# Kernel tuning notes

Hardware: AMD Instinct MI355X
Metric: run time of the kernel (lower is better)

The kernel has to match this reference:

```python
import jax, jax.numpy as jnp
import numpy as np

# (dy, dx) offsets corresponding to the single -1 entries of kernels 1..8
# delta1 rows: (0,0),(0,1),(0,2),(1,2); delta2 = spatial flip: (2,2),(2,1),(2,0),(1,0)
OFFSETS = [(-1, -1), (-1, 0), (-1, 1), (0, 1), (1, 1), (1, 0), (1, -1), (0, -1)]
NUM_LAYER = 9
EPS = 1e-12


def _shift(x, dy, dx):
    # zero-padded shift: out[y, x] = in[y + dy, x + dx]; dilation = shifts[0] = 1
    b, c, h, w = x.shape
    p = jnp.pad(x, ((0, 0), (0, 0), (1, 1), (1, 1)))
    return jax.lax.dynamic_slice(p, (0, 0, 1 + dy, 1 + dx), (b, c, h, w))


def _l2norm(v, axis):
    # matches torch.nn.functional.normalize: v / max(||v||, eps)
    n = jnp.sqrt(jnp.sum(v * v, axis=axis, keepdims=True))
    return v / jnp.maximum(n, EPS)


def setup_inputs() -> dict:
    key = jax.random.key(0)
    k1, k2, k3, k4 = jax.random.split(key, 4)
    B, C, H, W = 4, 256, 96, 96
    cen = jax.random.normal(k1, (B, C, H, W), dtype=jnp.float32)
    scale = 1.0 / np.sqrt(C)
    # grouped 1x1 convs (groups=9): per-group (C x C) weight matrices
    W1 = jax.random.normal(k2, (NUM_LAYER, C, C), dtype=jnp.float32) * scale
    W2 = jax.random.normal(k3, (C, C), dtype=jnp.float32) * scale
    W3 = jax.random.normal(k4, (NUM_LAYER, C, C), dtype=jnp.float32) * scale
    return {"cen": cen, "W1": W1, "W2": W2, "W3": W3}


def reference(cen, W1, W2, W3):
    b, c, h, w = cen.shape
    # Extract_layer: 8 fixed depthwise 3x3 convs (each = negated shift) + identity
    surrounds = jnp.stack(
        [-_shift(cen, dy, dx) for dy, dx in OFFSETS] + [cen], axis=1
    )  # (b, 9, c, h, w)
    # Analyze_layer: grouped 1x1 convs = per-group matmuls
    out1 = jnp.einsum("gij,bgjhw->bgihw", W1, surrounds)
    out2 = jnp.einsum("ij,bjhw->bihw", W2, cen)[:, None]  # (b, 1, c, h, w)
    out3 = jnp.einsum("gij,bgjhw->bgihw", W3, surrounds)
    out1 = _l2norm(out1, axis=2)
    out2 = _l2norm(out2, axis=2)
    out3 = _l2norm(out3, axis=2)
    # softmax over a size-1 axis (dim=2 after mean+keepdim) -> identically 1.0
    att = jax.nn.softmax(
        jnp.mean(out1 * out2, axis=2, keepdims=True), axis=2
    )  # (b, 9, 1, h, w)
    out = jnp.sum(att * out3, axis=1)  # (b, c, h, w)
    return out + cen
```

## Files before the change

### kernel.cpp

```cpp
#include <hip/hip_runtime.h>
#include <stdint.h>

#define BB 4
#define CC 256
#define HH 96
#define WW 96
#define HP 98
#define CP 264
#define XT 32
#define YT 2
#define XE 34

typedef __bf16 bf16x8 __attribute__((ext_vector_type(8)));
typedef float f32x4 __attribute__((ext_vector_type(4)));
typedef float f32x16 __attribute__((ext_vector_type(16)));

__device__ __forceinline__ uint16_t f2bf(float f) {
    uint32_t u = __float_as_uint(f);
    u += 0x7FFFu + ((u >> 16) & 1u);
    return (uint16_t)(u >> 16);
}

__global__ void transpose_cen(const float* __restrict__ cen, uint16_t* __restrict__ cenT) {
    const int y = blockIdx.x, b = blockIdx.y, ch = blockIdx.z, tid = threadIdx.x;
    __shared__ uint16_t ldsX[128 * 100];

    #pragma unroll
    for (int i = 0; i < 12; ++i) {
        int f = i * 256 + tid;
        int c = f / 24, xq = f % 24;
        float4 v = *(const float4*)(cen + ((((size_t)b * CC + ch * 128 + c) * HH + y) * WW + xq * 4));
        uint2 pk;
        pk.x = (uint32_t)f2bf(v.x) | ((uint32_t)f2bf(v.y) << 16);
        pk.y = (uint32_t)f2bf(v.z) | ((uint32_t)f2bf(v.w) << 16);
        *(uint2*)(&ldsX[c * 100 + xq * 4]) = pk;
    }
    __syncthreads();
    #pragma unroll
    for (int i = 0; i < 6; ++i) {
        int t = i * 256 + tid;
        int x = t % 96, cq = t / 96;
        uint32_t w0, w1, w2, w3;
        w0 = (uint32_t)ldsX[(cq * 8 + 0) * 100 + x] | ((uint32_t)ldsX[(cq * 8 + 1) * 100 + x] << 16);
        w1 = (uint32_t)ldsX[(cq * 8 + 2) * 100 + x] | ((uint32_t)ldsX[(cq * 8 + 3) * 100 + x] << 16);
        w2 = (uint32_t)ldsX[(cq * 8 + 4) * 100 + x] | ((uint32_t)ldsX[(cq * 8 + 5) * 100 + x] << 16);
        w3 = (uint32_t)ldsX[(cq * 8 + 6) * 100 + x] | ((uint32_t)ldsX[(cq * 8 + 7) * 100 + x] << 16);
        size_t o = (((size_t)b * HP + (y + 1)) * HP + (x + 1)) * CP + ch * 128 + cq * 8;
        *(uint4*)(cenT + o) = make_uint4(w0, w1, w2, w3);
    }
}

__global__ void cvt_w3(const float* __restrict__ W3, uint16_t* __restrict__ W3bf) {
    int e = (blockIdx.x * 256 + threadIdx.x) * 4;
    int g = e >> 16, n = (e >> 8) & 255, k = e & 255;
    float4 v = *(const float4*)(W3 + e);
    uint2 pk;
    pk.x = (uint32_t)f2bf(v.x) | ((uint32_t)f2bf(v.y) << 16);
    pk.y = (uint32_t)f2bf(v.z) | ((uint32_t)f2bf(v.w) << 16);
    size_t o = (size_t)(((g * 8 + (n >> 5)) * 16 + (k >> 4)) * 512)
             + (n & 31) * 16 + ((k >> 3) & 1) * 8 + (k & 7);
    *(uint2*)(W3bf + o) = pk;
}

__global__ __launch_bounds__(512, 4)
void ecm_main(const float* __restrict__ cen, const uint16_t* __restrict__ cenT,
              const uint16_t* __restrict__ W3bf, float* __restrict__ out) {
    const int tid = threadIdx.x;
    const int wv = tid >> 6, lane = tid & 63, col = lane & 31, kh = lane >> 5;
    const int x0 = blockIdx.x * XT, y0 = blockIdx.y * YT, b = blockIdx.z;

    __shared__ __align__(16) uint16_t ldsA[YT * XE * CP];
    __shared__ __align__(16) float ldsP[2][64][8];

    const int dgOrd[9] = {0, 1, 2, 7, 8, 3, 6, 5, 4};

    const uint16_t* wbase = W3bf + (size_t)wv * 16 * 512 + col * 16 + kh * 8;
    f32x16 fin0 = {}, fin1 = {};

    #pragma unroll 1
    for (int idx = 0; idx < 9; ++idx) {
        const int g = dgOrd[idx], dg = idx / 3, dx = idx % 3 - 1;

        if (idx % 3 == 0) {
            for (int r = 0; r < YT; ++r) {
                const uint4* gs = (const uint4*)(cenT + (((size_t)b * HP + (y0 + dg + r)) * HP + x0) * CP);
                uint4* ls = (uint4*)(ldsA + r * XE * CP);
                for (int c = tid; c < XE * CP / 8; c += 512) ls[c] = gs[c];
            }
            __syncthreads();
        }

        const uint16_t* wg = wbase + (size_t)g * 65536;
        const int a0 = (col + dx + 1) * CP + kh * 8;
        const int a1 = a0 + XE * CP;

        f32x16 acc0 = {}, acc1 = {};
        bf16x8 wf = *(const bf16x8*)(wg);
        bf16x8 b0 = *(const bf16x8*)(ldsA + a0);
        bf16x8 b1 = *(const bf16x8*)(ldsA + a1);
        #pragma unroll
        for (int ks = 0; ks < 15; ++ks) {
            bf16x8 wn  = *(const bf16x8*)(wg + (ks + 1) * 512);
            bf16x8 bn0 = *(const bf16x8*)(ldsA + a0 + (ks + 1) * 16);
            bf16x8 bn1 = *(const bf16x8*)(ldsA + a1 + (ks + 1) * 16);
            acc0 = __builtin_amdgcn_mfma_f32_32x32x16_bf16(wf, b0, acc0, 0, 0, 0);
            acc1 = __builtin_amdgcn_mfma_f32_32x32x16_bf16(wf, b1, acc1, 0, 0, 0);
            wf = wn; b0 = bn0; b1 = bn1;
        }
        acc0 = __builtin_amdgcn_mfma_f32_32x32x16_bf16(wf, b0, acc0, 0, 0, 0);
        acc1 = __builtin_amdgcn_mfma_f32_32x32x16_bf16(wf, b1, acc1, 0, 0, 0);

        float s0 = 0.f, s1 = 0.f;
        #pragma unroll
        for (int r = 0; r < 16; ++r) { s0 += acc0[r] * acc0[r]; s1 += acc1[r] * acc1[r]; }
        s0 += __shfl_xor(s0, 32, 64);
        s1 += __shfl_xor(s1, 32, 64);
        if (kh == 0) { ldsP[idx & 1][col][wv] = s0; ldsP[idx & 1][32 + col][wv] = s1; }
        __syncthreads();

        f32x4 pa = *(const f32x4*)&ldsP[idx & 1][col][0];
        f32x4 pb = *(const f32x4*)&ldsP[idx & 1][col][4];
        f32x4 qa = *(const f32x4*)&ldsP[idx & 1][32 + col][0];
        f32x4 qb = *(const f32x4*)&ldsP[idx & 1][32 + col][4];
        float n0 = pa[0] + pa[1] + pa[2] + pa[3] + pb[0] + pb[1] + pb[2] + pb[3];
        float n1 = qa[0] + qa[1] + qa[2] + qa[3] + qb[0] + qb[1] + qb[2] + qb[3];
        const float sgn = (g == 8) ? 1.f : -1.f;
        float sc0 = sgn / fmaxf(sqrtf(n0), 1e-12f);
        float sc1 = sgn / fmaxf(sqrtf(n1), 1e-12f);
        #pragma unroll
        for (int r = 0; r < 16; ++r) { fin0[r] += acc0[r] * sc0; fin1[r] += acc1[r] * sc1; }
    }

    #pragma unroll
    for (int r = 0; r < 16; ++r) {
        int ch = wv * 32 + (r & 3) + 8 * (r >> 2) + 4 * kh;
        size_t o0 = (((size_t)b * CC + ch) * HH + y0) * WW + (x0 + col);
        size_t o1 = o0 + WW;
        out[o0] = fin0[r] + cen[o0];
        out[o1] = fin1[r] + cen[o1];
    }
}

extern "C" void kernel_launch(void* const* d_in, const int* in_sizes, int n_in,
                              void* d_out, int out_size, void* d_ws, size_t ws_size,
                              hipStream_t stream) {
    const float* cen = (const float*)d_in[0];
    const float* W3 = (const float*)d_in[3];
    float* out = (float*)d_out;

    uint16_t* cenT = (uint16_t*)d_ws;
    const size_t cenT_elems = (size_t)BB * HP * HP * CP;
    uint16_t* W3bf = cenT + cenT_elems;

    hipMemsetAsync(d_ws, 0, cenT_elems * sizeof(uint16_t), stream);
    transpose_cen<<<dim3(HH, BB, 2), 256, 0, stream>>>(cen, cenT);
    cvt_w3<<<576, 256, 0, stream>>>(W3, W3bf);
    ecm_main<<<dim3(3, 48, 4), 512, 0, stream>>>(cen, cenT, W3bf, out);
}
```

Measured before the change: 180.6 us.

## Shrink main kernel tile to one row per block to raise occupancy

Each block of the main kernel now handles one output row instead of two, which halves the shared-memory tile and the accumulator registers. The grid doubles along y, and the launch bounds now allow 6 blocks per SM instead of 4. The aim is more resident waves and less register/LDS pressure. The cost is that each weight fragment is loaded once per row instead of being reused across two rows, which doubles weight traffic, and the manual software prefetch of the K loop is replaced by a plain unroll-2 loop.

Result: slower. 204.6 us (+13.3%).

```diff
diff --git a/kernel.cpp b/kernel.cpp
--- a/kernel.cpp
+++ b/kernel.cpp
@@ -8,7 +8,6 @@
 #define HP 98
 #define CP 264
 #define XT 32
-#define YT 2
 #define XE 34
 
 typedef __bf16 bf16x8 __attribute__((ext_vector_type(8)));
@@ -62,82 +61,66 @@
     *(uint2*)(W3bf + o) = pk;
 }
 
-__global__ __launch_bounds__(512, 4)
+__global__ __launch_bounds__(512, 6)
 void ecm_main(const float* __restrict__ cen, const uint16_t* __restrict__ cenT,
               const uint16_t* __restrict__ W3bf, float* __restrict__ out) {
     const int tid = threadIdx.x;
     const int wv = tid >> 6, lane = tid & 63, col = lane & 31, kh = lane >> 5;
-    const int x0 = blockIdx.x * XT, y0 = blockIdx.y * YT, b = blockIdx.z;
+    const int x0 = blockIdx.x * XT, y = blockIdx.y, b = blockIdx.z;
 
-    __shared__ __align__(16) uint16_t ldsA[YT * XE * CP];
-    __shared__ __align__(16) float ldsP[2][64][8];
+    __shared__ __align__(16) uint16_t ldsA[XE * CP];
+    __shared__ __align__(16) float ldsP[2][32][8];
 
     const int dgOrd[9] = {0, 1, 2, 7, 8, 3, 6, 5, 4};
 
-    const uint16_t* wbase = W3bf + (size_t)wv * 16 * 512 + col * 16 + kh * 8;
-    f32x16 fin0 = {}, fin1 = {};
+    const uint16_t* wbase = W3bf + (size_t)wv * (16 * 512) + col * 16 + kh * 8;
+    const int abase = col * CP + kh * 8;
+
+    f32x16 fin = {};
 
     #pragma unroll 1
     for (int idx = 0; idx < 9; ++idx) {
         const int g = dgOrd[idx], dg = idx / 3, dx = idx % 3 - 1;
 
         if (idx % 3 == 0) {
-            for (int r = 0; r < YT; ++r) {
-                const uint4* gs = (const uint4*)(cenT + (((size_t)b * HP + (y0 + dg + r)) * HP + x0) * CP);
-                uint4* ls = (uint4*)(ldsA + r * XE * CP);
-                for (int c = tid; c < XE * CP / 8; c += 512) ls[c] = gs[c];
-            }
+            const uint4* gs = (const uint4*)(cenT + (((size_t)b * HP + (y + dg)) * HP + x0) * CP);
+            uint4* ls = (uint4*)ldsA;
+            for (int c = tid; c < XE * CP / 8; c += 512) ls[c] = gs[c];
             __syncthreads();
         }
 
-        const uint16_t* wg = wbase + (size_t)g * 65536;
-        const int a0 = (col + dx + 1) * CP + kh * 8;
-        const int a1 = a0 + XE * CP;
+        const uint16_t* wg = wbase + (size_t)g * (8 * 16 * 512);
+        const int a = abase + (dx + 1) * CP;
 
-        f32x16 acc0 = {}, acc1 = {};
-        bf16x8 wf = *(const bf16x8*)(wg);
-        bf16x8 b0 = *(const bf16x8*)(ldsA + a0);
-        bf16x8 b1 = *(const bf16x8*)(ldsA + a1);
+        f32x16 acc = {};
+        #pragma unroll 2
+        for (int ks = 0; ks < 16; ++ks) {
+            bf16x8 wf = *(const bf16x8*)(wg + ks * 512);
+            bf16x8 bf = *(const bf16x8*)(ldsA + a + ks * 16);
+            acc = __builtin_amdgcn_mfma_f32_32x32x16_bf16(wf, bf, acc, 0, 0, 0);
+        }
+
+        float s = 0.f;
         #pragma unroll
-        for (int ks = 0; ks < 15; ++ks) {
-            bf16x8 wn  = *(const bf16x8*)(wg + (ks + 1) * 512);
-            bf16x8 bn0 = *(const bf16x8*)(ldsA + a0 + (ks + 1) * 16);
-            bf16x8 bn1 = *(const bf16x8*)(ldsA + a1 + (ks + 1) * 16);
-            acc0 = __builtin_amdgcn_mfma_f32_32x32x16_bf16(wf, b0, acc0, 0, 0, 0);
-            acc1 = __builtin_amdgcn_mfma_f32_32x32x16_bf16(wf, b1, acc1, 0, 0, 0);
-            wf = wn; b0 = bn0; b1 = bn1;
-        }
-        acc0 = __builtin_amdgcn_mfma_f32_32x32x16_bf16(wf, b0, acc0, 0, 0, 0);
-        acc1 = __builtin_amdgcn_mfma_f32_32x32x16_bf16(wf, b1, acc1, 0, 0, 0);
-
-        float s0 = 0.f, s1 = 0.f;
-        #pragma unroll
-        for (int r = 0; r < 16; ++r) { s0 += acc0[r] * acc0[r]; s1 += acc1[r] * acc1[r]; }
-        s0 += __shfl_xor(s0, 32, 64);
-        s1 += __shfl_xor(s1, 32, 64);
-        if (kh == 0) { ldsP[idx & 1][col][wv] = s0; ldsP[idx & 1][32 + col][wv] = s1; }
+        for (int r = 0; r < 16; ++r) s += acc[r] * acc[r];
+        s += __shfl_xor(s, 32, 64);
+        if (kh == 0) ldsP[idx & 1][col][wv] = s;
         __syncthreads();
 
         f32x4 pa = *(const f32x4*)&ldsP[idx & 1][col][0];
         f32x4 pb = *(const f32x4*)&ldsP[idx & 1][col][4];
-        f32x4 qa = *(const f32x4*)&ldsP[idx & 1][32 + col][0];
-        f32x4 qb = *(const f32x4*)&ldsP[idx & 1][32 + col][4];
-        float n0 = pa[0] + pa[1] + pa[2] + pa[3] + pb[0] + pb[1] + pb[2] + pb[3];
-        float n1 = qa[0] + qa[1] + qa[2] + qa[3] + qb[0] + qb[1] + qb[2] + qb[3];
+        float n = pa[0] + pa[1] + pa[2] + pa[3] + pb[0] + pb[1] + pb[2] + pb[3];
         const float sgn = (g == 8) ? 1.f : -1.f;
-        float sc0 = sgn / fmaxf(sqrtf(n0), 1e-12f);
-        float sc1 = sgn / fmaxf(sqrtf(n1), 1e-12f);
+        float sc = sgn / fmaxf(sqrtf(n), 1e-12f);
         #pragma unroll
-        for (int r = 0; r < 16; ++r) { fin0[r] += acc0[r] * sc0; fin1[r] += acc1[r] * sc1; }
+        for (int r = 0; r < 16; ++r) fin[r] += acc[r] * sc;
     }
 
     #pragma unroll
     for (int r = 0; r < 16; ++r) {
         int ch = wv * 32 + (r & 3) + 8 * (r >> 2) + 4 * kh;
-        size_t o0 = (((size_t)b * CC + ch) * HH + y0) * WW + (x0 + col);
-        size_t o1 = o0 + WW;
-        out[o0] = fin0[r] + cen[o0];
-        out[o1] = fin1[r] + cen[o1];
+        size_t o = (((size_t)b * CC + ch) * HH + y) * WW + (x0 + col);
+        out[o] = fin[r] + cen[o];
     }
 }
 
@@ -155,5 +138,5 @@
     hipMemsetAsync(d_ws, 0, cenT_elems * sizeof(uint16_t), stream);
     transpose_cen<<<dim3(HH, BB, 2), 256, 0, stream>>>(cen, cenT);
     cvt_w3<<<576, 256, 0, stream>>>(W3, W3bf);
-    ecm_main<<<dim3(3, 48, 4), 512, 0, stream>>>(cen, cenT, W3bf, out);
+    ecm_main<<<dim3(3, HH, BB), 512, 0, stream>>>(cen, cenT, W3bf, out);
 }
```
